# Optimization experiments

Hardware: AMD Instinct MI355X
Metric: run time of the kernel (lower is better)

Reference implementation:

```python
import jax, jax.numpy as jnp
import numpy as np

BATCH, SIZE_IN, SIZE_OUT = 2048, 256, 512


def setup_inputs() -> dict:
    key = jax.random.key(0)
    kx, ka = jax.random.split(key)
    x = jax.random.normal(kx, (BATCH, SIZE_IN), dtype=jnp.float32)
    A = jax.random.normal(ka, (SIZE_IN, SIZE_OUT), dtype=jnp.float32)
    return {"x": x, "A": A}


def reference(x, A):
    # W = sigmoid(A): [size_in, size_out]
    W = jax.nn.sigmoid(A)
    # tropical (max-times) matmul: out[i,k] = max_j W[j,k] * x[i,j]
    # broadcast [B,1,J_in->axis1]... x: [B,J,1], W: [1,J,K] -> [B,J,K] -> max over J
    out = jnp.max(x[:, :, None] * W[None, :, :], axis=1)  # [B, K]
    return out
```

## Files before the change

### kernel.cpp

```cpp
#include <hip/hip_runtime.h>


typedef _Float16 h1;
typedef __attribute__((ext_vector_type(2))) _Float16 h2v;
typedef __attribute__((ext_vector_type(4))) float f4;
typedef __attribute__((ext_vector_type(8))) unsigned int u8v;

constexpr int JD = 256;
constexpr int KD = 512;

__device__ __forceinline__ float sigmoidf_fast(float a) {
    return 1.0f / (1.0f + __expf(-a));
}

__device__ __forceinline__ h2v asH2(unsigned int u) {
    union { unsigned int x; h2v h; } c; c.x = u; return c.h;
}

__global__ __launch_bounds__(256) void prepack(const float* __restrict__ x,
                                               const float* __restrict__ A,
                                               h2v* __restrict__ Wp,
                                               unsigned int* __restrict__ xp) {
    const int b = (int)blockIdx.x;
    if (b < 64) {
        const int t  = b * 256 + (int)threadIdx.x;
        const int p  = t >> 7;
        const int kq = (t & 127) << 2;
        const f4 a0 = *(const f4*)&A[(2 * p) * KD + kq];
        const f4 a1 = *(const f4*)&A[(2 * p + 1) * KD + kq];
        union { f4 v; h2v h[4]; } u;
        #pragma unroll
        for (int q = 0; q < 4; ++q)
            u.h[q] = h2v{(h1)sigmoidf_fast(a0[q]), (h1)sigmoidf_fast(a1[q])};
        *(f4*)&Wp[p * KD + kq] = u.v;
    } else {
        const int g = (b - 64) * 256 + (int)threadIdx.x;
        const f4 x0 = *(const f4*)&x[g * 8];
        const f4 x1 = *(const f4*)&x[g * 8 + 4];
        union { f4 v; h2v h[4]; } u;
        u.h[0] = h2v{(h1)x0.x, (h1)x0.y};
        u.h[1] = h2v{(h1)x0.z, (h1)x0.w};
        u.h[2] = h2v{(h1)x1.x, (h1)x1.y};
        u.h[3] = h2v{(h1)x1.z, (h1)x1.w};
        *(f4*)&xp[g * 4] = u.v;
    }
}

struct Chunk { u8v v0, v1, v2, v3; };

__device__ __forceinline__ void loadc(Chunk& C, const unsigned int* p) {
    C.v0 = *(const u8v*)(p);
    C.v1 = *(const u8v*)(p + 8);
    C.v2 = *(const u8v*)(p + 16);
    C.v3 = *(const u8v*)(p + 24);
}

__device__ __forceinline__ void compc(const Chunk& C, const h2v* wr, h2v& acc) {
    #pragma unroll
    for (int q = 0; q < 8; ++q) {
        acc = __builtin_elementwise_max(acc, asH2(C.v0[q]) * wr[q]);
        acc = __builtin_elementwise_max(acc, asH2(C.v1[q]) * wr[8 + q]);
        acc = __builtin_elementwise_max(acc, asH2(C.v2[q]) * wr[16 + q]);
        acc = __builtin_elementwise_max(acc, asH2(C.v3[q]) * wr[24 + q]);
    }
}

__global__ __launch_bounds__(256) void tropical_mm_kernel(
        const unsigned int* __restrict__ xp,
        const h2v* __restrict__ Wp,
        float* __restrict__ out) {
    const int lane = (int)threadIdx.x & 63;
    const int wv   = __builtin_amdgcn_readfirstlane((int)threadIdx.x >> 6);
    const int slab = (int)blockIdx.x & 7;
    const int rg   = (int)blockIdx.x >> 3;
    const int row0 = rg * 16 + wv * 4;
    const int k    = slab * 64 + lane;

    const unsigned int* xrow = xp + row0 * 128;

    h2v a0 = h2v{(h1)(-65504.0f), (h1)(-65504.0f)};
    h2v a1 = a0, a2 = a0, a3 = a0;

    Chunk A, B;

    #pragma unroll
    for (int H = 0; H < 2; ++H) {
        h2v wreg[64];
        #pragma unroll
        for (int p = 0; p < 64; ++p) wreg[p] = Wp[(H * 64 + p) * KD + k];

        const unsigned int* xb = xrow + H * 64;

        loadc(A, xb);
        loadc(B, xb + 32);        compc(A, wreg,      a0);
        loadc(A, xb + 128);       compc(B, wreg + 32, a0);
        loadc(B, xb + 128 + 32);  compc(A, wreg,      a1);
        loadc(A, xb + 256);       compc(B, wreg + 32, a1);
        loadc(B, xb + 256 + 32);  compc(A, wreg,      a2);
        loadc(A, xb + 384);       compc(B, wreg + 32, a2);
        loadc(B, xb + 384 + 32);  compc(A, wreg,      a3);
                                  compc(B, wreg + 32, a3);
    }

    out[(row0 + 0) * KD + k] = fmaxf((float)a0[0], (float)a0[1]);
    out[(row0 + 1) * KD + k] = fmaxf((float)a1[0], (float)a1[1]);
    out[(row0 + 2) * KD + k] = fmaxf((float)a2[0], (float)a2[1]);
    out[(row0 + 3) * KD + k] = fmaxf((float)a3[0], (float)a3[1]);
}

extern "C" void kernel_launch(void* const* d_in, const int* in_sizes, int n_in,
                              void* d_out, int out_size, void* d_ws, size_t ws_size,
                              hipStream_t stream) {
    const float* x = (const float*)d_in[0];
    const float* A = (const float*)d_in[1];
    float* out = (float*)d_out;

    h2v* Wp = (h2v*)d_ws;
    unsigned int* xp = (unsigned int*)((char*)d_ws + 256 * 1024);

    hipLaunchKernelGGL(prepack, dim3(320), dim3(256), 0, stream, x, A, Wp, xp);

    hipLaunchKernelGGL(tropical_mm_kernel, dim3(1024), dim3(256), 0, stream,
                       xp, Wp, out);
}
```

Baseline: 24.00 us.

## Stage W tile in LDS and stream x in chunks instead of register-caching W

The W prepack now groups four j-pairs per 16-byte element, so one wide load fetches eight j values for a column. The main kernel copies its 64-column W slab into shared memory once per block, then loops over 16 chunks, reading W from LDS and x from global with a 2x unroll. The old kernel held 64 W registers per half. The new one is meant to cut VGPR pressure and raise occupancy, at the cost of LDS reads and a block barrier.

```diff
diff --git a/kernel.cpp b/kernel.cpp
--- a/kernel.cpp
+++ b/kernel.cpp
@@ -4,7 +4,8 @@
 typedef _Float16 h1;
 typedef __attribute__((ext_vector_type(2))) _Float16 h2v;
 typedef __attribute__((ext_vector_type(4))) float f4;
-typedef __attribute__((ext_vector_type(8))) unsigned int u8v;
+typedef __attribute__((ext_vector_type(4))) unsigned int u4;
+typedef __attribute__((ext_vector_type(8))) unsigned int u8;
 
 constexpr int JD = 256;
 constexpr int KD = 512;
@@ -19,93 +20,89 @@
 
 __global__ __launch_bounds__(256) void prepack(const float* __restrict__ x,
                                                const float* __restrict__ A,
-                                               h2v* __restrict__ Wp,
-                                               unsigned int* __restrict__ xp) {
+                                               u4* __restrict__ Wq,
+                                               u4* __restrict__ xp4) {
     const int b = (int)blockIdx.x;
     if (b < 64) {
         const int t  = b * 256 + (int)threadIdx.x;
-        const int p  = t >> 7;
-        const int kq = (t & 127) << 2;
-        const f4 a0 = *(const f4*)&A[(2 * p) * KD + kq];
-        const f4 a1 = *(const f4*)&A[(2 * p + 1) * KD + kq];
-        union { f4 v; h2v h[4]; } u;
+        const int p4 = t >> 9;
+        const int k  = t & 511;
+        union { u4 v; h2v h[4]; } u;
         #pragma unroll
-        for (int q = 0; q < 4; ++q)
-            u.h[q] = h2v{(h1)sigmoidf_fast(a0[q]), (h1)sigmoidf_fast(a1[q])};
-        *(f4*)&Wp[p * KD + kq] = u.v;
+        for (int q = 0; q < 4; ++q) {
+            const float a0 = A[(8 * p4 + 2 * q) * KD + k];
+            const float a1 = A[(8 * p4 + 2 * q + 1) * KD + k];
+            u.h[q] = h2v{(h1)sigmoidf_fast(a0), (h1)sigmoidf_fast(a1)};
+        }
+        Wq[p4 * 512 + k] = u.v;
     } else {
         const int g = (b - 64) * 256 + (int)threadIdx.x;
         const f4 x0 = *(const f4*)&x[g * 8];
         const f4 x1 = *(const f4*)&x[g * 8 + 4];
-        union { f4 v; h2v h[4]; } u;
+        union { u4 v; h2v h[4]; } u;
         u.h[0] = h2v{(h1)x0.x, (h1)x0.y};
         u.h[1] = h2v{(h1)x0.z, (h1)x0.w};
         u.h[2] = h2v{(h1)x1.x, (h1)x1.y};
         u.h[3] = h2v{(h1)x1.z, (h1)x1.w};
-        *(f4*)&xp[g * 4] = u.v;
+        xp4[g] = u.v;
     }
 }
 
-struct Chunk { u8v v0, v1, v2, v3; };
+__global__ __launch_bounds__(256) void tropical_main(
+        const unsigned int* __restrict__ xp,
+        const u4* __restrict__ Wq,
+        float* __restrict__ out) {
+    __shared__ u4 Wl[32 * 64];
 
-__device__ __forceinline__ void loadc(Chunk& C, const unsigned int* p) {
-    C.v0 = *(const u8v*)(p);
-    C.v1 = *(const u8v*)(p + 8);
-    C.v2 = *(const u8v*)(p + 16);
-    C.v3 = *(const u8v*)(p + 24);
-}
-
-__device__ __forceinline__ void compc(const Chunk& C, const h2v* wr, h2v& acc) {
-    #pragma unroll
-    for (int q = 0; q < 8; ++q) {
-        acc = __builtin_elementwise_max(acc, asH2(C.v0[q]) * wr[q]);
-        acc = __builtin_elementwise_max(acc, asH2(C.v1[q]) * wr[8 + q]);
-        acc = __builtin_elementwise_max(acc, asH2(C.v2[q]) * wr[16 + q]);
-        acc = __builtin_elementwise_max(acc, asH2(C.v3[q]) * wr[24 + q]);
-    }
-}
-
-__global__ __launch_bounds__(256) void tropical_mm_kernel(
-        const unsigned int* __restrict__ xp,
-        const h2v* __restrict__ Wp,
-        float* __restrict__ out) {
-    const int lane = (int)threadIdx.x & 63;
-    const int wv   = __builtin_amdgcn_readfirstlane((int)threadIdx.x >> 6);
-    const int slab = (int)blockIdx.x & 7;
+    const int t    = (int)threadIdx.x;
+    const int lane = t & 63;
+    const int wv   = __builtin_amdgcn_readfirstlane(t >> 6);
+    const int kg   = (int)blockIdx.x & 7;
     const int rg   = (int)blockIdx.x >> 3;
-    const int row0 = rg * 16 + wv * 4;
-    const int k    = slab * 64 + lane;
-
-    const unsigned int* xrow = xp + row0 * 128;
-
-    h2v a0 = h2v{(h1)(-65504.0f), (h1)(-65504.0f)};
-    h2v a1 = a0, a2 = a0, a3 = a0;
-
-    Chunk A, B;
+    const int k0   = kg * 64;
+    const int r0   = rg * 16 + wv * 4;
 
     #pragma unroll
-    for (int H = 0; H < 2; ++H) {
-        h2v wreg[64];
+    for (int i = 0; i < 8; ++i) {
+        const int p4 = wv * 8 + i;
+        Wl[p4 * 64 + lane] = Wq[p4 * 512 + k0 + lane];
+    }
+    __syncthreads();
+
+    const unsigned int* xr = xp + r0 * 128;
+
+    h2v acc[4];
+    #pragma unroll
+    for (int r = 0; r < 4; ++r)
+        acc[r] = h2v{(h1)(-65504.0f), (h1)(-65504.0f)};
+
+    #pragma unroll 2
+    for (int c = 0; c < 16; ++c) {
+        u8 X[4];
         #pragma unroll
-        for (int p = 0; p < 64; ++p) wreg[p] = Wp[(H * 64 + p) * KD + k];
+        for (int r = 0; r < 4; ++r)
+            X[r] = *(const u8*)(xr + r * 128 + c * 8);
 
-        const unsigned int* xb = xrow + H * 64;
+        union { u4 v; h2v h[4]; } w0, w1;
+        w0.v = Wl[(2 * c + 0) * 64 + lane];
+        w1.v = Wl[(2 * c + 1) * 64 + lane];
 
-        loadc(A, xb);
-        loadc(B, xb + 32);        compc(A, wreg,      a0);
-        loadc(A, xb + 128);       compc(B, wreg + 32, a0);
-        loadc(B, xb + 128 + 32);  compc(A, wreg,      a1);
-        loadc(A, xb + 256);       compc(B, wreg + 32, a1);
-        loadc(B, xb + 256 + 32);  compc(A, wreg,      a2);
-        loadc(A, xb + 384);       compc(B, wreg + 32, a2);
-        loadc(B, xb + 384 + 32);  compc(A, wreg,      a3);
-                                  compc(B, wreg + 32, a3);
+        #pragma unroll
+        for (int r = 0; r < 4; ++r) {
+            #pragma unroll
+            for (int q = 0; q < 4; ++q) {
+                acc[r] = __builtin_elementwise_max(acc[r],
+                                                   asH2(X[r][q]) * w0.h[q]);
+                acc[r] = __builtin_elementwise_max(acc[r],
+                                                   asH2(X[r][4 + q]) * w1.h[q]);
+            }
+        }
     }
 
-    out[(row0 + 0) * KD + k] = fmaxf((float)a0[0], (float)a0[1]);
-    out[(row0 + 1) * KD + k] = fmaxf((float)a1[0], (float)a1[1]);
-    out[(row0 + 2) * KD + k] = fmaxf((float)a2[0], (float)a2[1]);
-    out[(row0 + 3) * KD + k] = fmaxf((float)a3[0], (float)a3[1]);
+    const int k = k0 + lane;
+    #pragma unroll
+    for (int r = 0; r < 4; ++r)
+        out[(r0 + r) * KD + k] = fmaxf((float)acc[r][0], (float)acc[r][1]);
 }
 
 extern "C" void kernel_launch(void* const* d_in, const int* in_sizes, int n_in,
@@ -115,11 +112,11 @@
     const float* A = (const float*)d_in[1];
     float* out = (float*)d_out;
 
-    h2v* Wp = (h2v*)d_ws;
-    unsigned int* xp = (unsigned int*)((char*)d_ws + 256 * 1024);
+    u4* Wq  = (u4*)d_ws;
+    u4* xp4 = (u4*)((char*)d_ws + 256 * 1024);
 
-    hipLaunchKernelGGL(prepack, dim3(320), dim3(256), 0, stream, x, A, Wp, xp);
+    hipLaunchKernelGGL(prepack, dim3(320), dim3(256), 0, stream, x, A, Wq, xp4);
 
-    hipLaunchKernelGGL(tropical_mm_kernel, dim3(1024), dim3(256), 0, stream,
-                       xp, Wp, out);
+    hipLaunchKernelGGL(tropical_main, dim3(1024), dim3(256), 0, stream,
+                       (const unsigned int*)xp4, Wq, out);
 }
```

After: 21.70 us. -9.6%, faster.
